# Kernel optimization log

Measured on AMD Instinct MI355X. Metric: run time of the kernel, lower is better.

The kernel has to match this reference:

```python
import jax, jax.numpy as jnp
import numpy as np

B, N, D, H, FF = 2, 2048, 768, 12, 3072
HD = D // H
RADIUS = 2.0
COORD_DIM = 3
LN_EPS = 1e-5


def _layernorm(x, g, b):
    m = jnp.mean(x, axis=-1, keepdims=True)
    v = jnp.mean((x - m) ** 2, axis=-1, keepdims=True)
    return (x - m) * jax.lax.rsqrt(v + LN_EPS) * g + b


def setup_inputs() -> dict:
    key = jax.random.key(0)
    ks = jax.random.split(key, 16)
    s = 0.02
    return {
        "x": jax.random.normal(ks[0], (B, N, D), jnp.float32),
        "coords": jax.random.uniform(ks[1], (B, N, COORD_DIM), jnp.float32) * 10.0,
        "w_qkv": jax.random.normal(ks[2], (D, 3 * D), jnp.float32) * s,
        "b_qkv": jnp.zeros((3 * D,), jnp.float32),
        "w_out": jax.random.normal(ks[3], (D, D), jnp.float32) * s,
        "b_out": jnp.zeros((D,), jnp.float32),
        "w_ff1": jax.random.normal(ks[4], (D, FF), jnp.float32) * s,
        "b_ff1": jnp.zeros((FF,), jnp.float32),
        "w_ff2": jax.random.normal(ks[5], (FF, D), jnp.float32) * s,
        "b_ff2": jnp.zeros((D,), jnp.float32),
        "g1": jnp.ones((D,), jnp.float32),
        "beta1": jnp.zeros((D,), jnp.float32),
        "g2": jnp.ones((D,), jnp.float32),
        "beta2": jnp.zeros((D,), jnp.float32),
    }


def reference(x, coords, w_qkv, b_qkv, w_out, b_out, w_ff1, b_ff1,
              w_ff2, b_ff2, g1, beta1, g2, beta2):
    # --- attention sub-block ---
    residual = x
    xn = _layernorm(x, g1, beta1)
    qkv = xn @ w_qkv + b_qkv                       # [B,N,3D]
    qkv = qkv.reshape(B, N, 3, H, HD)
    q, k, v = qkv[:, :, 0], qkv[:, :, 1], qkv[:, :, 2]   # [B,N,H,HD]

    # geometric radius mask: attend only to tokens within Euclidean RADIUS
    d2 = jnp.sum((coords[:, :, None, :] - coords[:, None, :, :]) ** 2, axis=-1)  # [B,N,N]
    mask = d2 <= RADIUS * RADIUS                   # self-distance 0 -> always true

    scores = jnp.einsum("bqhd,bkhd->bhqk", q, k) / jnp.sqrt(jnp.float32(HD))
    scores = jnp.where(mask[:, None, :, :], scores, jnp.float32(-1e9))
    attn = jax.nn.softmax(scores, axis=-1)
    attn_out = jnp.einsum("bhqk,bkhd->bqhd", attn, v).reshape(B, N, D)
    attn_out = attn_out @ w_out + b_out            # dropout=0 (eval)
    x = residual + attn_out

    # --- FFN sub-block ---
    residual = x
    xn = _layernorm(x, g2, beta2)
    h = jax.nn.gelu(xn @ w_ff1 + b_ff1, approximate=False)
    ff_out = h @ w_ff2 + b_ff2
    return residual + ff_out
```

## Files before the change

kernel.cpp:

```cpp
#include <hip/hip_runtime.h>
#include <hip/hip_bf16.h>

typedef unsigned short ushort_t;
typedef __attribute__((ext_vector_type(4))) float f32x4;
typedef __attribute__((ext_vector_type(8))) short s16x8;

#define DEV static __device__ __forceinline__

constexpr int Bb = 2, Nn = 2048, Dd = 768, Hh = 12, FFf = 3072;
constexpr int MTOK = Bb * Nn;
constexpr int QKVN = 3 * Dd;

DEV unsigned short f2bf(float f) {
    union { float f; unsigned int i; } x; x.f = f;
    unsigned int r = x.i + 0x7FFFu + ((x.i >> 16) & 1u);
    return (unsigned short)(r >> 16);
}

DEV void gload16(const void* g, void* l) {
    __builtin_amdgcn_global_load_lds(
        (const __attribute__((address_space(1))) void*)g,
        (__attribute__((address_space(3))) void*)l, 16, 0, 0);
}

DEV int xcd_swz(int lin, int n) {
    return (lin & 7) * (n >> 3) + (lin >> 3);
}

DEV float gelu_fast(float x) {
    float u = x * (0.7978845608f + 0.0356774081f * x * x);
    float e = __builtin_amdgcn_exp2f(2.885390082f * u);
    float th = 1.f - 2.f / (e + 1.f);
    return 0.5f * x * (1.f + th);
}

__global__ void k_transpose_all(const float* __restrict__ w_qkv, const float* __restrict__ w_out,
                                const float* __restrict__ w_ff1, const float* __restrict__ w_ff2,
                                unsigned short* __restrict__ o_qkv, unsigned short* __restrict__ o_out,
                                unsigned short* __restrict__ o_ff1, unsigned short* __restrict__ o_ff2) {
    __shared__ float t[32][33];
    int id = blockIdx.x;
    const float* in; unsigned short* out; int K, N, tid;
    if (id < 1728)      { in = w_qkv; out = o_qkv; K = 768;  N = 2304; tid = id; }
    else if (id < 2304) { in = w_out; out = o_out; K = 768;  N = 768;  tid = id - 1728; }
    else if (id < 4608) { in = w_ff1; out = o_ff1; K = 768;  N = 3072; tid = id - 2304; }
    else                { in = w_ff2; out = o_ff2; K = 3072; N = 768;  tid = id - 4608; }
    int nbx = N >> 5;
    int bx = (tid % nbx) * 32, by = (tid / nbx) * 32;
    int tx = threadIdx.x, ty = threadIdx.y;
#pragma unroll
    for (int i = 0; i < 4; i++)
        t[ty + 8 * i][tx] = in[(size_t)(by + ty + 8 * i) * N + bx + tx];
    __syncthreads();
#pragma unroll
    for (int i = 0; i < 4; i++)
        out[(size_t)(bx + ty + 8 * i) * K + by + tx] = f2bf(t[tx][ty + 8 * i]);
}

DEV int cell3(float x, float y, float z) {
    int cx = (int)(x * 0.5f); cx = cx > 4 ? 4 : cx;
    int cy = (int)(y * 0.5f); cy = cy > 4 ? 4 : cy;
    int cz = (int)(z * 0.5f); cz = cz > 4 ? 4 : cz;
    return (cz * 5 + cy) * 5 + cx;
}

__global__ __launch_bounds__(256) void k_sort(const float* __restrict__ coords,
                                              int* __restrict__ s2o,
                                              float4* __restrict__ c4s) {
    int b = blockIdx.y;
    int i = blockIdx.x * 4 + (threadIdx.x >> 6);
    int lane = threadIdx.x & 63;
    const float* cb = coords + (size_t)b * Nn * 3;
    float cix = cb[3 * i], ciy = cb[3 * i + 1], ciz = cb[3 * i + 2];
    int celli = cell3(cix, ciy, ciz);
    int pos = 0;
    for (int it = 0; it < Nn / 64; it++) {
        int j = it * 64 + lane;
        int cj = cell3(cb[3 * j], cb[3 * j + 1], cb[3 * j + 2]);
        bool before = (cj < celli) || (cj == celli && j < i);
        pos += __popcll(__ballot(before));
    }
    if (lane == 0) {
        s2o[b * Nn + pos] = i;
        c4s[b * Nn + pos] = make_float4(cix, ciy, ciz, 0.f);
    }
}

__global__ __launch_bounds__(256) void k_mask(const float4* __restrict__ c4s,
                                              unsigned long long* __restrict__ mb) {
    int qt = blockIdx.x, ks = blockIdx.y, b = blockIdx.z;
    __shared__ float4 ck[256];
    int t = threadIdx.x;
    ck[t] = c4s[b * Nn + ks * 256 + t];
    __syncthreads();
    int r = t >> 2, c = t & 3;
    int q = qt * 64 + r;
    float4 cq = c4s[b * Nn + q];
    unsigned long long w = 0;
#pragma unroll 8
    for (int j = 0; j < 64; j++) {
        float4 k4 = ck[c * 64 + j];
        float dx = __fsub_rn(cq.x, k4.x);
        float dy = __fsub_rn(cq.y, k4.y);
        float dz = __fsub_rn(cq.z, k4.z);
        float d2 = __fadd_rn(__fadd_rn(__fmul_rn(dx, dx), __fmul_rn(dy, dy)),
                             __fmul_rn(dz, dz));
        if (d2 <= 4.0f) w |= 1ull << j;
    }
    mb[((size_t)(b * Nn + q) << 5) + ks * 4 + c] = w;
}

__global__ __launch_bounds__(64) void k_tiles(const unsigned long long* __restrict__ mb,
                                              int* __restrict__ tl) {
    int q64 = blockIdx.x, b = blockIdx.y;
    int lane = threadIdx.x;
    unsigned long long v = 0;
    if (lane < 32) {
        const unsigned long long* base = mb + ((size_t)(b * Nn + q64 * 64) << 5) + lane;
        for (int r = 0; r < 64; r++) v |= base[(size_t)r << 5];
    }
    unsigned long long nz = __ballot(v != 0);
    int idx = __popcll(nz & ((1ull << lane) - 1));
    int* o = tl + (b * 32 + q64) * 33;
    if (v != 0) o[1 + idx] = lane;
    if (lane == 0) o[0] = __popcll(nz);
}

__global__ __launch_bounds__(128) void k_gatherK(const unsigned short* __restrict__ qkv,
                                                 const int* __restrict__ s2o,
                                                 unsigned short* __restrict__ Ksort) {
    int ns = blockIdx.x & (Nn - 1);
    int b = blockIdx.x >> 11;
    int t = threadIdx.x;
    int orig = s2o[b * Nn + ns];
    const s16x8* src = (const s16x8*)(qkv + ((size_t)b * Nn + orig) * QKVN + Dd);
    s16x8* dst = (s16x8*)(Ksort + ((size_t)b * Nn + ns) * Dd);
    if (t < 96) dst[t] = src[t];
}

__global__ __launch_bounds__(256) void k_vt(const unsigned short* __restrict__ qkv,
                                            const int* __restrict__ s2o,
                                            unsigned short* __restrict__ VtT) {
    __shared__ unsigned short Ld[64][72];
    int ns0 = blockIdx.x * 64;
    int bh = blockIdx.y;
    int b = bh / Hh, h = bh % Hh;
    int t = threadIdx.x;
#pragma unroll
    for (int i = 0; i < 2; i++) {
        int item = t + 256 * i;
        int row = item >> 3, ch = (item & 7) * 8;
        int orig = s2o[b * Nn + ns0 + row];
        *(s16x8*)&Ld[row][ch] =
            *(const s16x8*)(qkv + ((size_t)b * Nn + orig) * QKVN + 2 * Dd + h * 64 + ch);
    }
    __syncthreads();
    int vd = (t >> 5) * 8, vkp = (t & 31) * 2;
#pragma unroll
    for (int j = 0; j < 8; j++) {
        unsigned int pack = (unsigned int)Ld[vkp][vd + j] |
                            ((unsigned int)Ld[vkp + 1][vd + j] << 16);
        *(unsigned int*)((char*)VtT +
                         (((size_t)bh * 64 + vd + j) * Nn + ns0 + vkp) * 2) = pack;
    }
}

DEV float wred_sum(float v) {
#pragma unroll
    for (int o = 32; o; o >>= 1) v += __shfl_down(v, o, 64);
    return v;
}

__global__ __launch_bounds__(256) void k_ln(const float* __restrict__ x,
                                            const float* __restrict__ g,
                                            const float* __restrict__ be,
                                            unsigned short* __restrict__ out) {
    int row = blockIdx.x;
    const float* xr = x + (size_t)row * Dd;
    int t = threadIdx.x;
    float v0 = xr[t], v1 = xr[t + 256], v2 = xr[t + 512];
    float s = v0 + v1 + v2;
    float sq = v0 * v0 + v1 * v1 + v2 * v2;
    __shared__ float r1[4], r2[4];
    float ws = wred_sum(s), wq = wred_sum(sq);
    int wid = t >> 6, lane = t & 63;
    if (lane == 0) { r1[wid] = ws; r2[wid] = wq; }
    __syncthreads();
    s = r1[0] + r1[1] + r1[2] + r1[3];
    sq = r2[0] + r2[1] + r2[2] + r2[3];
    float mean = s * (1.f / Dd);
    float var = sq * (1.f / Dd) - mean * mean;
    float rs = rsqrtf(var + 1e-5f);
    unsigned short* orow = out + (size_t)row * Dd;
    orow[t]       = f2bf((v0 - mean) * rs * g[t]       + be[t]);
    orow[t + 256] = f2bf((v1 - mean) * rs * g[t + 256] + be[t + 256]);
    orow[t + 512] = f2bf((v2 - mean) * rs * g[t + 512] + be[t + 512]);
}

#define GEMM_PIPE_LOOP(NT)                                                              \
    stage(0, 0);                                                                        \
    if ((NT) > 1) stage(1, 1);                                                          \
    for (int t = 0; t < (NT); t++) {                                                    \
        int cur = t % 3;                                                                \
        if (t + 2 < (NT)) {                                                             \
            stage((t + 2) % 3, t + 2);                                                  \
            asm volatile("s_waitcnt vmcnt(8)" ::: "memory");                            \
        } else if (t + 1 < (NT)) {                                                      \
            asm volatile("s_waitcnt vmcnt(4)" ::: "memory");                            \
        } else {                                                                        \
            asm volatile("s_waitcnt vmcnt(0)" ::: "memory");                            \
        }                                                                               \
        __builtin_amdgcn_sched_barrier(0);                                              \
        __builtin_amdgcn_s_barrier();                                                   \
        const unsigned short* Ab = As[cur];                                             \
        const unsigned short* Bbp = Bs[cur];                                            \
        s16x8 af[4], bfr[4];                                                            \
        _Pragma("unroll")                                                               \
        for (int i = 0; i < 4; i++) {                                                   \
            af[i]  = *(const s16x8*)&Ab[(wr * 64 + i * 16 + lr) * 32 + lg * 8];         \
            bfr[i] = *(const s16x8*)&Bbp[(wc * 64 + i * 16 + lr) * 32 + lg * 8];        \
        }                                                                               \
        _Pragma("unroll")                                                               \
        for (int mi = 0; mi < 4; mi++)                                                  \
            _Pragma("unroll")                                                           \
            for (int ni = 0; ni < 4; ni++)                                              \
                acc[mi][ni] = __builtin_amdgcn_mfma_f32_16x16x32_bf16(                  \
                    af[mi], bfr[ni], acc[mi][ni], 0, 0, 0);                             \
        __builtin_amdgcn_s_barrier();                                                   \
    }

template <int EPI>
__global__ __launch_bounds__(256) void k_gemm(const unsigned short* __restrict__ A,
                                              const unsigned short* __restrict__ Bt,
                                              const float* __restrict__ bias,
                                              const float* __restrict__ res,
                                              void* __restrict__ outp,
                                              int M, int N, int K) {
    constexpr int BM = 128, BN = 128, BK = 32;
    __shared__ unsigned short As[3][BM * BK];
    __shared__ unsigned short Bs[3][BN * BK];
    int NB = N >> 7;
    int id = xcd_swz(blockIdx.x, gridDim.x);
    int m0 = (id / NB) * BM, n0 = (id % NB) * BN;
    int t = threadIdx.x;
    int wid = t >> 6, lane = t & 63;
    int wr = wid >> 1, wc = wid & 1;
    int lg = lane >> 4, lr = lane & 15;
    f32x4 acc[4][4] = {};

    int srow = wid * 32 + (lane >> 2);
    int scol = (lane & 3) * 8;
    const unsigned short* Ag = A + (size_t)(m0 + srow) * K + scol;
    const unsigned short* Bg = Bt + (size_t)(n0 + srow) * K + scol;

    auto stage = [&](int buf, int kt) {
        int k0 = kt * BK;
        char* Al = (char*)As[buf] + wid * 2048;
        char* Bl = (char*)Bs[buf] + wid * 2048;
        gload16(Ag + k0, Al);
        gload16(Ag + k0 + (size_t)16 * K, Al + 1024);
        gload16(Bg + k0, Bl);
        gload16(Bg + k0 + (size_t)16 * K, Bl + 1024);
    };
    int nt = K / BK;
    GEMM_PIPE_LOOP(nt)

    int mrow = m0 + wr * 64;
    int ncol = n0 + wc * 64;
#pragma unroll
    for (int mi = 0; mi < 4; mi++) {
#pragma unroll
        for (int ni = 0; ni < 4; ni++) {
            int nn = ncol + ni * 16 + lr;
            float bs = bias[nn];
#pragma unroll
            for (int r = 0; r < 4; r++) {
                int mm = mrow + mi * 16 + lg * 4 + r;
                float v = acc[mi][ni][r] + bs;
                if (EPI == 1) {
                    ((unsigned short*)outp)[(size_t)mm * N + nn] = f2bf(gelu_fast(v));
                } else if (EPI == 2) {
                    v += res[(size_t)mm * N + nn];
                    ((float*)outp)[(size_t)mm * N + nn] = v;
                } else {
                    ((unsigned short*)outp)[(size_t)mm * N + nn] = f2bf(v);
                }
            }
        }
    }
}

template <int SPLIT>
__global__ __launch_bounds__(256) void k_gemm_sk(const unsigned short* __restrict__ A,
                                                 const unsigned short* __restrict__ Bt,
                                                 float* __restrict__ part,
                                                 int M, int N, int K) {
    constexpr int BM = 128, BN = 128, BK = 32;
    __shared__ unsigned short As[3][BM * BK];
    __shared__ unsigned short Bs[3][BN * BK];
    int NB = N >> 7, MB = M >> 7;
    int id = xcd_swz(blockIdx.x, gridDim.x);
    int nb = id % NB;
    int mbk = (id / NB) % MB;
    int kz = id / (NB * MB);
    int m0 = mbk * BM, n0 = nb * BN;
    int Kc = K / SPLIT, kb = kz * (Kc / BK);
    int t = threadIdx.x;
    int wid = t >> 6, lane = t & 63;
    int wr = wid >> 1, wc = wid & 1;
    int lg = lane >> 4, lr = lane & 15;
    f32x4 acc[4][4] = {};

    int srow = wid * 32 + (lane >> 2);
    int scol = (lane & 3) * 8;
    const unsigned short* Ag = A + (size_t)(m0 + srow) * K + scol;
    const unsigned short* Bg = Bt + (size_t)(n0 + srow) * K + scol;

    auto stage = [&](int buf, int kt) {
        int k0 = (kb + kt) * BK;
        char* Al = (char*)As[buf] + wid * 2048;
        char* Bl = (char*)Bs[buf] + wid * 2048;
        gload16(Ag + k0, Al);
        gload16(Ag + k0 + (size_t)16 * K, Al + 1024);
        gload16(Bg + k0, Bl);
        gload16(Bg + k0 + (size_t)16 * K, Bl + 1024);
    };
    int nt = Kc / BK;
    GEMM_PIPE_LOOP(nt)

    float* po = part + (size_t)kz * M * N;
    int mrow = m0 + wr * 64;
    int ncol = n0 + wc * 64;
#pragma unroll
    for (int mi = 0; mi < 4; mi++)
#pragma unroll
        for (int ni = 0; ni < 4; ni++) {
            int nn = ncol + ni * 16 + lr;
#pragma unroll
            for (int r = 0; r < 4; r++) {
                int mm = mrow + mi * 16 + lg * 4 + r;
                po[(size_t)mm * N + nn] = acc[mi][ni][r];
            }
        }
}

__global__ __launch_bounds__(256) void k_reduce4_ln(const float* __restrict__ part,
                                                    const float* __restrict__ bias,
                                                    const float* __restrict__ res,
                                                    const float* __restrict__ g,
                                                    const float* __restrict__ be,
                                                    float* __restrict__ x2,
                                                    unsigned short* __restrict__ xn,
                                                    int MN) {
    int wid = threadIdx.x >> 6, lane = threadIdx.x & 63;
    int row = blockIdx.x * 4 + wid;
    size_t base = (size_t)row * Dd;
    f32x4 v[3];
    float s = 0.f, sq = 0.f;
#pragma unroll
    for (int j = 0; j < 3; j++) {
        int col = j * 256 + lane * 4;
        f32x4 a0 = *(const f32x4*)(part + base + col);
        f32x4 a1 = *(const f32x4*)(part + (size_t)MN + base + col);
        f32x4 a2 = *(const f32x4*)(part + 2 * (size_t)MN + base + col);
        f32x4 a3 = *(const f32x4*)(part + 3 * (size_t)MN + base + col);
        f32x4 r = *(const f32x4*)(res + base + col);
        f32x4 bs = *(const f32x4*)(bias + col);
#pragma unroll
        for (int q = 0; q < 4; q++) {
            v[j][q] = (a0[q] + a1[q]) + (a2[q] + a3[q]) + bs[q] + r[q];
            s += v[j][q];
            sq += v[j][q] * v[j][q];
        }
        *(f32x4*)(x2 + base + col) = v[j];
    }
    s = wred_sum(s); sq = wred_sum(sq);
    s = __shfl(s, 0, 64); sq = __shfl(sq, 0, 64);
    float mean = s * (1.f / Dd);
    float var = sq * (1.f / Dd) - mean * mean;
    float rs = rsqrtf(var + 1e-5f);
#pragma unroll
    for (int j = 0; j < 3; j++) {
        int col = j * 256 + lane * 4;
        f32x4 gg = *(const f32x4*)(g + col);
        f32x4 bb = *(const f32x4*)(be + col);
        ushort4 o;
        o.x = f2bf((v[j][0] - mean) * rs * gg[0] + bb[0]);
        o.y = f2bf((v[j][1] - mean) * rs * gg[1] + bb[1]);
        o.z = f2bf((v[j][2] - mean) * rs * gg[2] + bb[2]);
        o.w = f2bf((v[j][3] - mean) * rs * gg[3] + bb[3]);
        *(ushort4*)(xn + base + col) = o;
    }
}

__global__ __launch_bounds__(256) void k_reduce4(const float* __restrict__ part,
                                                 const float* __restrict__ bias,
                                                 const float* __restrict__ res,
                                                 float* __restrict__ out,
                                                 int MN, int N) {
    int i = (blockIdx.x * 256 + threadIdx.x) * 4;
    f32x4 a0 = *(const f32x4*)(part + i);
    f32x4 a1 = *(const f32x4*)(part + (size_t)MN + i);
    f32x4 a2 = *(const f32x4*)(part + 2 * (size_t)MN + i);
    f32x4 a3 = *(const f32x4*)(part + 3 * (size_t)MN + i);
    f32x4 r = *(const f32x4*)(res + i);
    f32x4 bs = *(const f32x4*)(bias + (i % N));
    f32x4 o;
#pragma unroll
    for (int j = 0; j < 4; j++) o[j] = (a0[j] + a1[j]) + (a2[j] + a3[j]) + bs[j] + r[j];
    *(f32x4*)(out + i) = o;
}

constexpr float SC2 = 0.125f * 1.44269504088896340736f;
constexpr float PMASK = -3.0e38f;
constexpr float MINIT = -1.0e30f;

__global__ __launch_bounds__(256) void k_attn(const unsigned short* __restrict__ qkv,
                                              const unsigned short* __restrict__ Ksort,
                                              const unsigned short* __restrict__ VtT,
                                              const int* __restrict__ s2o,
                                              const uint2* __restrict__ mb,
                                              const int* __restrict__ tl,
                                              unsigned short* __restrict__ out) {
    int lin = blockIdx.x;
    int id = (lin & 7) * 96 + (lin >> 3);
    int q64 = id & 31;
    int hb = id >> 5;
    int h = hb % Hh, b = hb / Hh;
    int bh = b * Hh + h;

    __shared__ __align__(16) char sm[2 * 16384 + 4 * 2048];

    int t = threadIdx.x, wid = t >> 6, lane = t & 63;
    int lg = lane >> 4, lr = lane & 15;
    int sw = lr & 7;
    int qbase = q64 * 64 + wid * 16;

    int oq = s2o[b * Nn + qbase + lr];
    const unsigned short* Qb = qkv + ((size_t)b * Nn + oq) * QKVN + h * 64;
    s16x8 qf0 = *(const s16x8*)(Qb + lg * 8);
    s16x8 qf1 = *(const s16x8*)(Qb + 32 + lg * 8);

    const uint2* mrow = mb + ((size_t)(b * Nn + qbase + lr) << 5);
    const int* tle = tl + (b * 32 + q64) * 33;
    int tlv = (lane < 33) ? tle[lane] : 0;
    int cnt = __shfl(tlv, 0, 64);

    int srow = lane >> 3, sch = lane & 7;
    int krow = wid * 8 + srow;
    int kx = sch ^ (krow & 7);
    const unsigned short* Kg0 = Ksort + ((size_t)b * Nn + krow) * Dd + h * 64 + kx * 8;
    const unsigned short* Vg0 = VtT + ((size_t)bh * 64 + krow) * Nn + kx * 8;
    char* pw = sm + 32768 + wid * 2048 + lr * 128;

    float m2 = MINIT, l_run = 0.f;
    f32x4 oacc[4] = {};

    int tid0 = __shfl(tlv, 1, 64);
    uint2 Mw = mrow[tid0];
    {
        char* Kl = sm + wid * 1024;
        gload16(Kg0 + (size_t)(tid0 * 64) * Dd, Kl);
        gload16(Kg0 + (size_t)(tid0 * 64 + 32) * Dd, Kl + 4096);
        char* Vl = sm + 8192 + wid * 1024;
        gload16(Vg0 + tid0 * 64, Vl);
        gload16(Vg0 + tid0 * 64 + 32 * (size_t)Nn, Vl + 4096);
    }
    __syncthreads();

    for (int ti = 0; ti < cnt; ti++) {
        int cur = ti & 1;
        uint2 MwN;
        if (ti + 1 < cnt) {
            int tidn = __shfl(tlv, 2 + ti, 64);
            char* Kl = sm + (cur ^ 1) * 16384 + wid * 1024;
            gload16(Kg0 + (size_t)(tidn * 64) * Dd, Kl);
            gload16(Kg0 + (size_t)(tidn * 64 + 32) * Dd, Kl + 4096);
            char* Vl = sm + (cur ^ 1) * 16384 + 8192 + wid * 1024;
            gload16(Vg0 + tidn * 64, Vl);
            gload16(Vg0 + tidn * 64 + 32 * (size_t)Nn, Vl + 4096);
            MwN = mrow[tidn];
        }

        if (__any((Mw.x | Mw.y) != 0)) {
            const char* Kbuf = sm + cur * 16384;
            const char* Vbuf = Kbuf + 8192;

            __builtin_amdgcn_s_setprio(1);
            f32x4 st[4];
#pragma unroll
            for (int s = 0; s < 4; s++) {
                const char* kr = Kbuf + (s * 16 + lr) * 128;
                s16x8 kf0 = *(const s16x8*)(kr + ((lg ^ sw) << 4));
                s16x8 kf1 = *(const s16x8*)(kr + (((4 + lg) ^ sw) << 4));
                f32x4 z = {};
                z = __builtin_amdgcn_mfma_f32_16x16x32_bf16(kf0, qf0, z, 0, 0, 0);
                st[s] = __builtin_amdgcn_mfma_f32_16x16x32_bf16(kf1, qf1, z, 0, 0, 0);
            }
            __builtin_amdgcn_s_setprio(0);

            float p[4][4];
            float mt = PMASK;
#pragma unroll
            for (int s = 0; s < 4; s++) {
                unsigned int wsel = (s < 2) ? Mw.x : Mw.y;
#pragma unroll
                for (int r = 0; r < 4; r++) {
                    float sv = st[s][r] * SC2;
                    unsigned int bit = (wsel >> ((s & 1) * 16 + lg * 4 + r)) & 1u;
                    p[s][r] = bit ? sv : PMASK;
                    mt = fmaxf(mt, p[s][r]);
                }
            }
            mt = fmaxf(mt, __shfl_xor(mt, 16, 64));
            mt = fmaxf(mt, __shfl_xor(mt, 32, 64));

            if (!__all(mt <= m2 + 11.5416f)) {
                float mn2 = fmaxf(m2, mt);
                float fac = __builtin_amdgcn_exp2f(m2 - mn2);
                l_run *= fac;
                m2 = mn2;
                float fr[4];
#pragma unroll
                for (int r = 0; r < 4; r++) fr[r] = __shfl(fac, (lane & 48) + lg * 4 + r, 64);
#pragma unroll
                for (int dt = 0; dt < 4; dt++)
#pragma unroll
                    for (int r = 0; r < 4; r++) oacc[dt][r] *= fr[r];
            }

            float lt = 0.f;
#pragma unroll
            for (int s = 0; s < 4; s++)
#pragma unroll
                for (int r = 0; r < 4; r++) {
                    p[s][r] = __builtin_amdgcn_exp2f(p[s][r] - m2);
                    lt += p[s][r];
                }
            lt += __shfl_xor(lt, 16, 64);
            lt += __shfl_xor(lt, 32, 64);
            l_run += lt;

#pragma unroll
            for (int s = 0; s < 4; s++) {
                unsigned int lo = (unsigned int)f2bf(p[s][0]) | ((unsigned int)f2bf(p[s][1]) << 16);
                unsigned int hi = (unsigned int)f2bf(p[s][2]) | ((unsigned int)f2bf(p[s][3]) << 16);
                unsigned long long u = (unsigned long long)lo | ((unsigned long long)hi << 32);
                int chunk = (s * 2 + (lg >> 1)) ^ sw;
                *(unsigned long long*)(pw + (chunk << 4) + (lg & 1) * 8) = u;
            }

            __builtin_amdgcn_s_setprio(1);
#pragma unroll
            for (int c = 0; c < 2; c++) {
                s16x8 pf = *(const s16x8*)(pw + (((c * 4 + lg) ^ sw) << 4));
#pragma unroll
                for (int dt = 0; dt < 4; dt++) {
                    const char* vr = Vbuf + (dt * 16 + lr) * 128;
                    s16x8 vf = *(const s16x8*)(vr + (((c * 4 + lg) ^ sw) << 4));
                    oacc[dt] = __builtin_amdgcn_mfma_f32_16x16x32_bf16(pf, vf, oacc[dt], 0, 0, 0);
                }
            }
            __builtin_amdgcn_s_setprio(0);
        }

        __syncthreads();
        Mw = MwN;
    }

    float lr4[4];
    int orow[4];
#pragma unroll
    for (int r = 0; r < 4; r++) {
        lr4[r] = __shfl(l_run, (lane & 48) + lg * 4 + r, 64);
        orow[r] = s2o[b * Nn + qbase + lg * 4 + r];
    }
#pragma unroll
    for (int dt = 0; dt < 4; dt++)
#pragma unroll
        for (int r = 0; r < 4; r++) {
            float v = oacc[dt][r] / lr4[r];
            out[((size_t)b * Nn + orow[r]) * Dd + h * 64 + dt * 16 + lr] = f2bf(v);
        }
}

extern "C" void kernel_launch(void* const* d_in, const int* in_sizes, int n_in,
                              void* d_out, int out_size, void* d_ws, size_t ws_size,
                              hipStream_t stream) {
    const float* x      = (const float*)d_in[0];
    const float* coords = (const float*)d_in[1];
    const float* w_qkv  = (const float*)d_in[2];
    const float* b_qkv  = (const float*)d_in[3];
    const float* w_out  = (const float*)d_in[4];
    const float* b_out  = (const float*)d_in[5];
    const float* w_ff1  = (const float*)d_in[6];
    const float* b_ff1  = (const float*)d_in[7];
    const float* w_ff2  = (const float*)d_in[8];
    const float* b_ff2  = (const float*)d_in[9];
    const float* g1     = (const float*)d_in[10];
    const float* beta1  = (const float*)d_in[11];
    const float* g2     = (const float*)d_in[12];
    const float* beta2  = (const float*)d_in[13];

    char* ws = (char*)d_ws;
    size_t off = 0;
    auto alloc = [&](size_t bytes) {
        char* p = ws + off;
        off += (bytes + 255) & ~(size_t)255;
        return p;
    };
    unsigned short* w_qkv_t = (unsigned short*)alloc((size_t)QKVN * Dd * 2);
    unsigned short* w_out_t = (unsigned short*)alloc((size_t)Dd * Dd * 2);
    unsigned short* w_ff1_t = (unsigned short*)alloc((size_t)FFf * Dd * 2);
    unsigned short* w_ff2_t = (unsigned short*)alloc((size_t)Dd * FFf * 2);
    float4*         c4s     = (float4*)alloc((size_t)MTOK * 16);
    int*            s2o     = (int*)alloc((size_t)MTOK * 4);
    unsigned long long* mbits = (unsigned long long*)alloc((size_t)MTOK * 32 * 8);
    int*            tl      = (int*)alloc((size_t)Bb * 32 * 33 * 4);
    unsigned short* xn      = (unsigned short*)alloc((size_t)MTOK * Dd * 2);
    unsigned short* hbuf    = (unsigned short*)alloc((size_t)MTOK * FFf * 2);
    float*          x2      = (float*)alloc((size_t)MTOK * Dd * 4);
    unsigned short* attn_o  = (unsigned short*)alloc((size_t)MTOK * Dd * 2);
    unsigned short* qkv     = (unsigned short*)alloc((size_t)MTOK * QKVN * 2);
    unsigned short* Ksort   = (unsigned short*)alloc((size_t)MTOK * Dd * 2);
    unsigned short* VtT     = (unsigned short*)alloc((size_t)Bb * Hh * 64 * Nn * 2);
    float*          partial = (float*)alloc((size_t)4 * MTOK * Dd * 4);

    k_transpose_all<<<dim3(6912), dim3(32, 8), 0, stream>>>(
        w_qkv, w_out, w_ff1, w_ff2, w_qkv_t, w_out_t, w_ff1_t, w_ff2_t);
    k_sort<<<dim3(Nn / 4, Bb), 256, 0, stream>>>(coords, s2o, c4s);
    k_mask<<<dim3(Nn / 64, 8, Bb), 256, 0, stream>>>(c4s, mbits);
    k_tiles<<<dim3(32, Bb), 64, 0, stream>>>(mbits, tl);

    k_ln<<<MTOK, 256, 0, stream>>>(x, g1, beta1, xn);
    k_gemm<0><<<dim3((QKVN / 128) * (MTOK / 128)), 256, 0, stream>>>(
        xn, w_qkv_t, b_qkv, nullptr, qkv, MTOK, QKVN, Dd);
    k_gatherK<<<dim3(MTOK), 128, 0, stream>>>(qkv, s2o, Ksort);
    k_vt<<<dim3(Nn / 64, Bb * Hh), 256, 0, stream>>>(qkv, s2o, VtT);
    k_attn<<<dim3((Nn / 64) * Hh * Bb), 256, 0, stream>>>(
        qkv, Ksort, VtT, s2o, (const uint2*)mbits, tl, attn_o);
    k_gemm_sk<4><<<dim3((Dd / 128) * (MTOK / 128) * 4), 256, 0, stream>>>(
        attn_o, w_out_t, partial, MTOK, Dd, Dd);
    k_reduce4_ln<<<dim3(MTOK / 4), 256, 0, stream>>>(
        partial, b_out, x, g2, beta2, x2, xn, MTOK * Dd);
    k_gemm<1><<<dim3((FFf / 128) * (MTOK / 128)), 256, 0, stream>>>(
        xn, w_ff1_t, b_ff1, nullptr, hbuf, MTOK, FFf, Dd);
    k_gemm_sk<4><<<dim3((Dd / 128) * (MTOK / 128) * 4), 256, 0, stream>>>(
        hbuf, w_ff2_t, partial, MTOK, Dd, FFf);
    k_reduce4<<<dim3(MTOK * Dd / 1024), 256, 0, stream>>>(
        partial, b_ff2, x2, (float*)d_out, MTOK * Dd, Dd);
}
```

Measured before the change: 204.3 us.

## Replace 128x128 GEMM with 256x256 tile, 512-thread kernel for QKV and FF1

After: 226.6 us. 10.9% more time.

```diff
diff --git a/kernel.cpp b/kernel.cpp
--- a/kernel.cpp
+++ b/kernel.cpp
@@ -195,6 +195,93 @@
     orow[t]       = f2bf((v0 - mean) * rs * g[t]       + be[t]);
     orow[t + 256] = f2bf((v1 - mean) * rs * g[t + 256] + be[t + 256]);
     orow[t + 512] = f2bf((v2 - mean) * rs * g[t + 512] + be[t + 512]);
+}
+
+template <int EPI>
+__global__ __launch_bounds__(512, 2) void k_gemm256(const unsigned short* __restrict__ A,
+                                                    const unsigned short* __restrict__ Bt,
+                                                    const float* __restrict__ bias,
+                                                    unsigned short* __restrict__ outp,
+                                                    int M, int N, int K) {
+    constexpr int BM = 256, BN = 256, BK = 32;
+    __shared__ unsigned short As[3][BM * BK];
+    __shared__ unsigned short Bs[3][BN * BK];
+    int NB = N >> 8;
+    int id = xcd_swz(blockIdx.x, gridDim.x);
+    int m0 = (id / NB) * BM, n0 = (id % NB) * BN;
+    int t = threadIdx.x;
+    int wid = t >> 6, lane = t & 63;
+    int wr = wid >> 2, wc = wid & 3;
+    int lg = lane >> 4, lr = lane & 15;
+    f32x4 acc[8][4] = {};
+
+    int srow = t >> 2, sch = t & 3;
+    auto stage = [&](int buf, int kt) {
+        int k0 = kt * BK;
+#pragma unroll
+        for (int g = 0; g < 2; g++) {
+            int ar = g * 128 + srow;
+            gload16(A + (size_t)(m0 + ar) * K + k0 + ((sch ^ (ar & 3)) * 8),
+                    (char*)As[buf] + g * 8192 + wid * 1024);
+        }
+#pragma unroll
+        for (int g = 0; g < 2; g++) {
+            int br = g * 128 + srow;
+            gload16(Bt + (size_t)(n0 + br) * K + k0 + ((sch ^ (br & 3)) * 8),
+                    (char*)Bs[buf] + g * 8192 + wid * 1024);
+        }
+    };
+
+    int NT = K / BK;
+    stage(0, 0);
+    stage(1, 1);
+    for (int k = 0; k < NT; k++) {
+        int cur = k % 3;
+        if (k + 1 < NT) {
+            asm volatile("s_waitcnt vmcnt(4)" ::: "memory");
+        } else {
+            asm volatile("s_waitcnt vmcnt(0)" ::: "memory");
+        }
+        __builtin_amdgcn_sched_barrier(0);
+        __builtin_amdgcn_s_barrier();
+        __builtin_amdgcn_sched_barrier(0);
+        if (k + 2 < NT) stage((k + 2) % 3, k + 2);
+        s16x8 af[8], bfr[4];
+#pragma unroll
+        for (int i = 0; i < 8; i++) {
+            int row = wr * 128 + i * 16 + lr;
+            af[i] = *(const s16x8*)((const char*)As[cur] + row * 64 + ((lg ^ (row & 3)) << 4));
+        }
+#pragma unroll
+        for (int j = 0; j < 4; j++) {
+            int row = wc * 64 + j * 16 + lr;
+            bfr[j] = *(const s16x8*)((const char*)Bs[cur] + row * 64 + ((lg ^ (row & 3)) << 4));
+        }
+#pragma unroll
+        for (int i = 0; i < 8; i++)
+#pragma unroll
+            for (int j = 0; j < 4; j++)
+                acc[i][j] = __builtin_amdgcn_mfma_f32_16x16x32_bf16(
+                    af[i], bfr[j], acc[i][j], 0, 0, 0);
+    }
+
+    int mrow = m0 + wr * 128;
+    int ncol = n0 + wc * 64;
+#pragma unroll
+    for (int i = 0; i < 8; i++) {
+#pragma unroll
+        for (int j = 0; j < 4; j++) {
+            int nn = ncol + j * 16 + lr;
+            float bs = bias[nn];
+#pragma unroll
+            for (int r = 0; r < 4; r++) {
+                int mm = mrow + i * 16 + lg * 4 + r;
+                float v = acc[i][j][r] + bs;
+                if (EPI == 1) v = gelu_fast(v);
+                outp[(size_t)mm * N + nn] = f2bf(v);
+            }
+        }
+    }
 }
 
 #define GEMM_PIPE_LOOP(NT)                                                              \
@@ -229,67 +316,6 @@
         __builtin_amdgcn_s_barrier();                                                   \
     }
 
-template <int EPI>
-__global__ __launch_bounds__(256) void k_gemm(const unsigned short* __restrict__ A,
-                                              const unsigned short* __restrict__ Bt,
-                                              const float* __restrict__ bias,
-                                              const float* __restrict__ res,
-                                              void* __restrict__ outp,
-                                              int M, int N, int K) {
-    constexpr int BM = 128, BN = 128, BK = 32;
-    __shared__ unsigned short As[3][BM * BK];
-    __shared__ unsigned short Bs[3][BN * BK];
-    int NB = N >> 7;
-    int id = xcd_swz(blockIdx.x, gridDim.x);
-    int m0 = (id / NB) * BM, n0 = (id % NB) * BN;
-    int t = threadIdx.x;
-    int wid = t >> 6, lane = t & 63;
-    int wr = wid >> 1, wc = wid & 1;
-    int lg = lane >> 4, lr = lane & 15;
-    f32x4 acc[4][4] = {};
-
-    int srow = wid * 32 + (lane >> 2);
-    int scol = (lane & 3) * 8;
-    const unsigned short* Ag = A + (size_t)(m0 + srow) * K + scol;
-    const unsigned short* Bg = Bt + (size_t)(n0 + srow) * K + scol;
-
-    auto stage = [&](int buf, int kt) {
-        int k0 = kt * BK;
-        char* Al = (char*)As[buf] + wid * 2048;
-        char* Bl = (char*)Bs[buf] + wid * 2048;
-        gload16(Ag + k0, Al);
-        gload16(Ag + k0 + (size_t)16 * K, Al + 1024);
-        gload16(Bg + k0, Bl);
-        gload16(Bg + k0 + (size_t)16 * K, Bl + 1024);
-    };
-    int nt = K / BK;
-    GEMM_PIPE_LOOP(nt)
-
-    int mrow = m0 + wr * 64;
-    int ncol = n0 + wc * 64;
-#pragma unroll
-    for (int mi = 0; mi < 4; mi++) {
-#pragma unroll
-        for (int ni = 0; ni < 4; ni++) {
-            int nn = ncol + ni * 16 + lr;
-            float bs = bias[nn];
-#pragma unroll
-            for (int r = 0; r < 4; r++) {
-                int mm = mrow + mi * 16 + lg * 4 + r;
-                float v = acc[mi][ni][r] + bs;
-                if (EPI == 1) {
-                    ((unsigned short*)outp)[(size_t)mm * N + nn] = f2bf(gelu_fast(v));
-                } else if (EPI == 2) {
-                    v += res[(size_t)mm * N + nn];
-                    ((float*)outp)[(size_t)mm * N + nn] = v;
-                } else {
-                    ((unsigned short*)outp)[(size_t)mm * N + nn] = f2bf(v);
-                }
-            }
-        }
-    }
-}
-
 template <int SPLIT>
 __global__ __launch_bounds__(256) void k_gemm_sk(const unsigned short* __restrict__ A,
                                                  const unsigned short* __restrict__ Bt,
@@ -633,8 +659,8 @@
     k_tiles<<<dim3(32, Bb), 64, 0, stream>>>(mbits, tl);
 
     k_ln<<<MTOK, 256, 0, stream>>>(x, g1, beta1, xn);
-    k_gemm<0><<<dim3((QKVN / 128) * (MTOK / 128)), 256, 0, stream>>>(
-        xn, w_qkv_t, b_qkv, nullptr, qkv, MTOK, QKVN, Dd);
+    k_gemm256<0><<<dim3((MTOK / 256) * (QKVN / 256)), 512, 0, stream>>>(
+        xn, w_qkv_t, b_qkv, qkv, MTOK, QKVN, Dd);
     k_gatherK<<<dim3(MTOK), 128, 0, stream>>>(qkv, s2o, Ksort);
     k_vt<<<dim3(Nn / 64, Bb * Hh), 256, 0, stream>>>(qkv, s2o, VtT);
     k_attn<<<dim3((Nn / 64) * Hh * Bb), 256, 0, stream>>>(
@@ -643,8 +669,8 @@
         attn_o, w_out_t, partial, MTOK, Dd, Dd);
     k_reduce4_ln<<<dim3(MTOK / 4), 256, 0, stream>>>(
         partial, b_out, x, g2, beta2, x2, xn, MTOK * Dd);
-    k_gemm<1><<<dim3((FFf / 128) * (MTOK / 128)), 256, 0, stream>>>(
-        xn, w_ff1_t, b_ff1, nullptr, hbuf, MTOK, FFf, Dd);
+    k_gemm256<1><<<dim3((MTOK / 256) * (FFf / 256)), 512, 0, stream>>>(
+        xn, w_ff1_t, b_ff1, hbuf, MTOK, FFf, Dd);
     k_gemm_sk<4><<<dim3((Dd / 128) * (MTOK / 128) * 4), 256, 0, stream>>>(
         hbuf, w_ff2_t, partial, MTOK, Dd, FFf);
     k_reduce4<<<dim3(MTOK * Dd / 1024), 256, 0, stream>>>(
```

## Run whole block in coordinate-sorted token order, gather at LN and scatter at end

Applied to the files above, without the earlier changes.

After: 200.8 us. About the same (-1.7%).

```diff
diff --git a/kernel.cpp b/kernel.cpp
--- a/kernel.cpp
+++ b/kernel.cpp
@@ -126,20 +126,7 @@
     if (lane == 0) o[0] = __popcll(nz);
 }
 
-__global__ __launch_bounds__(128) void k_gatherK(const unsigned short* __restrict__ qkv,
-                                                 const int* __restrict__ s2o,
-                                                 unsigned short* __restrict__ Ksort) {
-    int ns = blockIdx.x & (Nn - 1);
-    int b = blockIdx.x >> 11;
-    int t = threadIdx.x;
-    int orig = s2o[b * Nn + ns];
-    const s16x8* src = (const s16x8*)(qkv + ((size_t)b * Nn + orig) * QKVN + Dd);
-    s16x8* dst = (s16x8*)(Ksort + ((size_t)b * Nn + ns) * Dd);
-    if (t < 96) dst[t] = src[t];
-}
-
 __global__ __launch_bounds__(256) void k_vt(const unsigned short* __restrict__ qkv,
-                                            const int* __restrict__ s2o,
                                             unsigned short* __restrict__ VtT) {
     __shared__ unsigned short Ld[64][72];
     int ns0 = blockIdx.x * 64;
@@ -150,9 +137,8 @@
     for (int i = 0; i < 2; i++) {
         int item = t + 256 * i;
         int row = item >> 3, ch = (item & 7) * 8;
-        int orig = s2o[b * Nn + ns0 + row];
         *(s16x8*)&Ld[row][ch] =
-            *(const s16x8*)(qkv + ((size_t)b * Nn + orig) * QKVN + 2 * Dd + h * 64 + ch);
+            *(const s16x8*)(qkv + ((size_t)b * Nn + ns0 + row) * QKVN + 2 * Dd + h * 64 + ch);
     }
     __syncthreads();
     int vd = (t >> 5) * 8, vkp = (t & 31) * 2;
@@ -171,12 +157,14 @@
     return v;
 }
 
-__global__ __launch_bounds__(256) void k_ln(const float* __restrict__ x,
-                                            const float* __restrict__ g,
-                                            const float* __restrict__ be,
-                                            unsigned short* __restrict__ out) {
+__global__ __launch_bounds__(256) void k_ln_g(const float* __restrict__ x,
+                                              const int* __restrict__ s2o,
+                                              const float* __restrict__ g,
+                                              const float* __restrict__ be,
+                                              unsigned short* __restrict__ out) {
     int row = blockIdx.x;
-    const float* xr = x + (size_t)row * Dd;
+    int orig = (row & ~(Nn - 1)) | s2o[row];
+    const float* xr = x + (size_t)orig * Dd;
     int t = threadIdx.x;
     float v0 = xr[t], v1 = xr[t + 256], v2 = xr[t + 512];
     float s = v0 + v1 + v2;
@@ -233,8 +221,7 @@
 __global__ __launch_bounds__(256) void k_gemm(const unsigned short* __restrict__ A,
                                               const unsigned short* __restrict__ Bt,
                                               const float* __restrict__ bias,
-                                              const float* __restrict__ res,
-                                              void* __restrict__ outp,
+                                              unsigned short* __restrict__ outp,
                                               int M, int N, int K) {
     constexpr int BM = 128, BN = 128, BK = 32;
     __shared__ unsigned short As[3][BM * BK];
@@ -277,14 +264,8 @@
             for (int r = 0; r < 4; r++) {
                 int mm = mrow + mi * 16 + lg * 4 + r;
                 float v = acc[mi][ni][r] + bs;
-                if (EPI == 1) {
-                    ((unsigned short*)outp)[(size_t)mm * N + nn] = f2bf(gelu_fast(v));
-                } else if (EPI == 2) {
-                    v += res[(size_t)mm * N + nn];
-                    ((float*)outp)[(size_t)mm * N + nn] = v;
-                } else {
-                    ((unsigned short*)outp)[(size_t)mm * N + nn] = f2bf(v);
-                }
+                if (EPI == 1) v = gelu_fast(v);
+                outp[(size_t)mm * N + nn] = f2bf(v);
             }
         }
     }
@@ -346,7 +327,8 @@
 
 __global__ __launch_bounds__(256) void k_reduce4_ln(const float* __restrict__ part,
                                                     const float* __restrict__ bias,
-                                                    const float* __restrict__ res,
+                                                    const float* __restrict__ x,
+                                                    const int* __restrict__ s2o,
                                                     const float* __restrict__ g,
                                                     const float* __restrict__ be,
                                                     float* __restrict__ x2,
@@ -354,7 +336,9 @@
                                                     int MN) {
     int wid = threadIdx.x >> 6, lane = threadIdx.x & 63;
     int row = blockIdx.x * 4 + wid;
+    int orig = (row & ~(Nn - 1)) | s2o[row];
     size_t base = (size_t)row * Dd;
+    size_t obase = (size_t)orig * Dd;
     f32x4 v[3];
     float s = 0.f, sq = 0.f;
 #pragma unroll
@@ -364,7 +348,7 @@
         f32x4 a1 = *(const f32x4*)(part + (size_t)MN + base + col);
         f32x4 a2 = *(const f32x4*)(part + 2 * (size_t)MN + base + col);
         f32x4 a3 = *(const f32x4*)(part + 3 * (size_t)MN + base + col);
-        f32x4 r = *(const f32x4*)(res + base + col);
+        f32x4 r = *(const f32x4*)(x + obase + col);
         f32x4 bs = *(const f32x4*)(bias + col);
 #pragma unroll
         for (int q = 0; q < 4; q++) {
@@ -393,22 +377,32 @@
     }
 }
 
-__global__ __launch_bounds__(256) void k_reduce4(const float* __restrict__ part,
-                                                 const float* __restrict__ bias,
-                                                 const float* __restrict__ res,
-                                                 float* __restrict__ out,
-                                                 int MN, int N) {
-    int i = (blockIdx.x * 256 + threadIdx.x) * 4;
-    f32x4 a0 = *(const f32x4*)(part + i);
-    f32x4 a1 = *(const f32x4*)(part + (size_t)MN + i);
-    f32x4 a2 = *(const f32x4*)(part + 2 * (size_t)MN + i);
-    f32x4 a3 = *(const f32x4*)(part + 3 * (size_t)MN + i);
-    f32x4 r = *(const f32x4*)(res + i);
-    f32x4 bs = *(const f32x4*)(bias + (i % N));
-    f32x4 o;
-#pragma unroll
-    for (int j = 0; j < 4; j++) o[j] = (a0[j] + a1[j]) + (a2[j] + a3[j]) + bs[j] + r[j];
-    *(f32x4*)(out + i) = o;
+__global__ __launch_bounds__(256) void k_reduce4_sc(const float* __restrict__ part,
+                                                    const float* __restrict__ bias,
+                                                    const float* __restrict__ res,
+                                                    const int* __restrict__ s2o,
+                                                    float* __restrict__ out,
+                                                    int MN) {
+    int wid = threadIdx.x >> 6, lane = threadIdx.x & 63;
+    int row = blockIdx.x * 4 + wid;
+    int orig = (row & ~(Nn - 1)) | s2o[row];
+    size_t base = (size_t)row * Dd;
+    size_t obase = (size_t)orig * Dd;
+#pragma unroll
+    for (int j = 0; j < 3; j++) {
+        int col = j * 256 + lane * 4;
+        f32x4 a0 = *(const f32x4*)(part + base + col);
+        f32x4 a1 = *(const f32x4*)(part + (size_t)MN + base + col);
+        f32x4 a2 = *(const f32x4*)(part + 2 * (size_t)MN + base + col);
+        f32x4 a3 = *(const f32x4*)(part + 3 * (size_t)MN + base + col);
+        f32x4 r = *(const f32x4*)(res + base + col);
+        f32x4 bs = *(const f32x4*)(bias + col);
+        f32x4 o;
+#pragma unroll
+        for (int q = 0; q < 4; q++)
+            o[q] = (a0[q] + a1[q]) + (a2[q] + a3[q]) + bs[q] + r[q];
+        *(f32x4*)(out + obase + col) = o;
+    }
 }
 
 constexpr float SC2 = 0.125f * 1.44269504088896340736f;
@@ -416,9 +410,7 @@
 constexpr float MINIT = -1.0e30f;
 
 __global__ __launch_bounds__(256) void k_attn(const unsigned short* __restrict__ qkv,
-                                              const unsigned short* __restrict__ Ksort,
                                               const unsigned short* __restrict__ VtT,
-                                              const int* __restrict__ s2o,
                                               const uint2* __restrict__ mb,
                                               const int* __restrict__ tl,
                                               unsigned short* __restrict__ out) {
@@ -436,8 +428,7 @@
     int sw = lr & 7;
     int qbase = q64 * 64 + wid * 16;
 
-    int oq = s2o[b * Nn + qbase + lr];
-    const unsigned short* Qb = qkv + ((size_t)b * Nn + oq) * QKVN + h * 64;
+    const unsigned short* Qb = qkv + ((size_t)b * Nn + qbase + lr) * QKVN + h * 64;
     s16x8 qf0 = *(const s16x8*)(Qb + lg * 8);
     s16x8 qf1 = *(const s16x8*)(Qb + 32 + lg * 8);
 
@@ -449,7 +440,7 @@
     int srow = lane >> 3, sch = lane & 7;
     int krow = wid * 8 + srow;
     int kx = sch ^ (krow & 7);
-    const unsigned short* Kg0 = Ksort + ((size_t)b * Nn + krow) * Dd + h * 64 + kx * 8;
+    const unsigned short* Kg0 = qkv + ((size_t)b * Nn + krow) * QKVN + Dd + h * 64 + kx * 8;
     const unsigned short* Vg0 = VtT + ((size_t)bh * 64 + krow) * Nn + kx * 8;
     char* pw = sm + 32768 + wid * 2048 + lr * 128;
 
@@ -460,8 +451,8 @@
     uint2 Mw = mrow[tid0];
     {
         char* Kl = sm + wid * 1024;
-        gload16(Kg0 + (size_t)(tid0 * 64) * Dd, Kl);
-        gload16(Kg0 + (size_t)(tid0 * 64 + 32) * Dd, Kl + 4096);
+        gload16(Kg0 + (size_t)(tid0 * 64) * QKVN, Kl);
+        gload16(Kg0 + (size_t)(tid0 * 64 + 32) * QKVN, Kl + 4096);
         char* Vl = sm + 8192 + wid * 1024;
         gload16(Vg0 + tid0 * 64, Vl);
         gload16(Vg0 + tid0 * 64 + 32 * (size_t)Nn, Vl + 4096);
@@ -474,8 +465,8 @@
         if (ti + 1 < cnt) {
             int tidn = __shfl(tlv, 2 + ti, 64);
             char* Kl = sm + (cur ^ 1) * 16384 + wid * 1024;
-            gload16(Kg0 + (size_t)(tidn * 64) * Dd, Kl);
-            gload16(Kg0 + (size_t)(tidn * 64 + 32) * Dd, Kl + 4096);
+            gload16(Kg0 + (size_t)(tidn * 64) * QKVN, Kl);
+            gload16(Kg0 + (size_t)(tidn * 64 + 32) * QKVN, Kl + 4096);
             char* Vl = sm + (cur ^ 1) * 16384 + 8192 + wid * 1024;
             gload16(Vg0 + tidn * 64, Vl);
             gload16(Vg0 + tidn * 64 + 32 * (size_t)Nn, Vl + 4096);
@@ -569,18 +560,15 @@
     }
 
     float lr4[4];
-    int orow[4];
-#pragma unroll
-    for (int r = 0; r < 4; r++) {
+#pragma unroll
+    for (int r = 0; r < 4; r++)
         lr4[r] = __shfl(l_run, (lane & 48) + lg * 4 + r, 64);
-        orow[r] = s2o[b * Nn + qbase + lg * 4 + r];
-    }
 #pragma unroll
     for (int dt = 0; dt < 4; dt++)
 #pragma unroll
         for (int r = 0; r < 4; r++) {
             float v = oacc[dt][r] / lr4[r];
-            out[((size_t)b * Nn + orow[r]) * Dd + h * 64 + dt * 16 + lr] = f2bf(v);
+            out[((size_t)b * Nn + qbase + lg * 4 + r) * Dd + h * 64 + dt * 16 + lr] = f2bf(v);
         }
 }
 
@@ -622,7 +610,6 @@
     float*          x2      = (float*)alloc((size_t)MTOK * Dd * 4);
     unsigned short* attn_o  = (unsigned short*)alloc((size_t)MTOK * Dd * 2);
     unsigned short* qkv     = (unsigned short*)alloc((size_t)MTOK * QKVN * 2);
-    unsigned short* Ksort   = (unsigned short*)alloc((size_t)MTOK * Dd * 2);
     unsigned short* VtT     = (unsigned short*)alloc((size_t)Bb * Hh * 64 * Nn * 2);
     float*          partial = (float*)alloc((size_t)4 * MTOK * Dd * 4);
 
@@ -632,21 +619,20 @@
     k_mask<<<dim3(Nn / 64, 8, Bb), 256, 0, stream>>>(c4s, mbits);
     k_tiles<<<dim3(32, Bb), 64, 0, stream>>>(mbits, tl);
 
-    k_ln<<<MTOK, 256, 0, stream>>>(x, g1, beta1, xn);
+    k_ln_g<<<MTOK, 256, 0, stream>>>(x, s2o, g1, beta1, xn);
     k_gemm<0><<<dim3((QKVN / 128) * (MTOK / 128)), 256, 0, stream>>>(
-        xn, w_qkv_t, b_qkv, nullptr, qkv, MTOK, QKVN, Dd);
-    k_gatherK<<<dim3(MTOK), 128, 0, stream>>>(qkv, s2o, Ksort);
-    k_vt<<<dim3(Nn / 64, Bb * Hh), 256, 0, stream>>>(qkv, s2o, VtT);
+        xn, w_qkv_t, b_qkv, qkv, MTOK, QKVN, Dd);
+    k_vt<<<dim3(Nn / 64, Bb * Hh), 256, 0, stream>>>(qkv, VtT);
     k_attn<<<dim3((Nn / 64) * Hh * Bb), 256, 0, stream>>>(
-        qkv, Ksort, VtT, s2o, (const uint2*)mbits, tl, attn_o);
+        qkv, VtT, (const uint2*)mbits, tl, attn_o);
     k_gemm_sk<4><<<dim3((Dd / 128) * (MTOK / 128) * 4), 256, 0, stream>>>(
         attn_o, w_out_t, partial, MTOK, Dd, Dd);
     k_reduce4_ln<<<dim3(MTOK / 4), 256, 0, stream>>>(
-        partial, b_out, x, g2, beta2, x2, xn, MTOK * Dd);
+        partial, b_out, x, s2o, g2, beta2, x2, xn, MTOK * Dd);
     k_gemm<1><<<dim3((FFf / 128) * (MTOK / 128)), 256, 0, stream>>>(
-        xn, w_ff1_t, b_ff1, nullptr, hbuf, MTOK, FFf, Dd);
+        xn, w_ff1_t, b_ff1, hbuf, MTOK, FFf, Dd);
     k_gemm_sk<4><<<dim3((Dd / 128) * (MTOK / 128) * 4), 256, 0, stream>>>(
         hbuf, w_ff2_t, partial, MTOK, Dd, FFf);
-    k_reduce4<<<dim3(MTOK * Dd / 1024), 256, 0, stream>>>(
-        partial, b_ff2, x2, (float*)d_out, MTOK * Dd, Dd);
-}
+    k_reduce4_sc<<<dim3(MTOK / 4), 256, 0, stream>>>(
+        partial, b_ff2, x2, s2o, (float*)d_out, MTOK * Dd);
+}
```
